# Performance work log

Measured on AMD Instinct MI355X. Metric: run time of the kernel, lower is better.

## Reference

```python
import jax, jax.numpy as jnp
import numpy as np

B, C, L, HEADS, DK = 32, 128, 32, 8, 64  # batch, channels, lattice side (L1=L2=L), heads, head dim
NLAYER = 4


def setup_inputs() -> dict:
    key = jax.random.key(0)
    ks = jax.random.split(key, 6)
    s_in = 1.0 / float(np.sqrt(C))          # lecun-normal scale for QKV (fan_in = channels)
    s_out = 1.0 / float(np.sqrt(HEADS * DK))  # lecun-normal scale for W0 (fan_in = dk*heads)
    return {
        "x": jax.random.normal(ks[0], (B, C, L, L), jnp.float32),
        "Wq": jax.random.normal(ks[1], (HEADS * DK, C), jnp.float32) * s_in,
        "Wk": jax.random.normal(ks[2], (HEADS * DK, C), jnp.float32) * s_in,
        "Wv": jax.random.normal(ks[3], (HEADS * DK, C), jnp.float32) * s_in,
        "R": jax.random.normal(ks[4], (HEADS, L, L), jnp.float32) * 0.02,
        "W0": jax.random.normal(ks[5], (C, HEADS * DK), jnp.float32) * s_out,
    }


def get_irpe(R):
    # r[h, i, j] = R[h, (xi - xj) mod L1, (yi - yj) mod L2]  (jnp negative indexing wraps)
    heads, L1, L2 = R.shape
    a1 = jnp.arange(L1)
    a2 = jnp.arange(L2)
    dx = (a1[:, None] - a1[None, :]) % L1        # (L1, L1)
    dy = (a2[:, None] - a2[None, :]) % L2        # (L2, L2)
    bias = R[:, dx[:, None, :, None], dy[None, :, None, :]]  # (heads, L1, L2, L1, L2)
    return bias.reshape(heads, L1 * L2, L1 * L2)


def reference(x, Wq, Wk, Wv, R, W0):
    bias = get_irpe(R)                            # (heads, N, N)
    inv_layer = 1.0 / float(np.sqrt(NLAYER + 1))
    inv_sqrt_dk = 1.0 / float(np.sqrt(DK))

    def block(xs):  # xs: (C, L, L) — single sample, as in the original __call__
        xn = xs * inv_layer
        xf = xn.reshape(C, -1)                    # (C, N)
        Q = (Wq @ xf).reshape(HEADS, DK, -1)      # 1x1 conv == matmul
        K = (Wk @ xf).reshape(HEADS, DK, -1)
        V = (Wv @ xf).reshape(HEADS, DK, -1)
        dot = jnp.einsum('hdi,hdj->hij', Q, K) + bias
        alpha = jax.nn.softmax(dot * inv_sqrt_dk, axis=-1)
        att = jnp.einsum('hij,hdj->hdi', alpha, V).reshape(HEADS * DK, -1)
        return (W0 @ att).reshape(xs.shape) + xs  # residual

    return jax.vmap(block)(x)
```

## Files before the change

### kernel.cpp

```cpp
#include <hip/hip_runtime.h>


#define NB   32
#define NH   8
#define SEQ  1024
#define DKH  64
#define HDIM 512
#define CIN  128

#define SCL 0.18033688011112042f

typedef __bf16 bf16x8 __attribute__((ext_vector_type(8)));
typedef float floatx4 __attribute__((ext_vector_type(4)));
typedef unsigned short u16x8 __attribute__((ext_vector_type(8)));
typedef unsigned int uintx4 __attribute__((ext_vector_type(4)));

__device__ __forceinline__ unsigned short f2bf(float f) {
    union { float f; unsigned int u; } c; c.f = f;
    unsigned int u = c.u;
    return (unsigned short)((u + 0x7fffu + ((u >> 16) & 1u)) >> 16);
}
__device__ __forceinline__ bf16x8 ldfrag(const unsigned short* p) {
    u16x8 v = *reinterpret_cast<const u16x8*>(p);
    return __builtin_bit_cast(bf16x8, v);
}
__device__ __forceinline__ unsigned int pkbf(float a, float b) {
    unsigned int ua = __builtin_bit_cast(unsigned int, a);
    unsigned int ub = __builtin_bit_cast(unsigned int, b);
    ua += 0x7fffu + ((ua >> 16) & 1u);
    ub += 0x7fffu + ((ub >> 16) & 1u);
    return __builtin_amdgcn_perm(ub, ua, 0x07060302u);
}
__device__ __forceinline__ unsigned int pkbf_t(float a, float b) {
    return __builtin_amdgcn_perm(__builtin_bit_cast(unsigned int, b),
                                 __builtin_bit_cast(unsigned int, a), 0x07060302u);
}


__global__ __launch_bounds__(256) void prep_wb(const float* __restrict__ Wq,
                                               const float* __restrict__ Wk,
                                               const float* __restrict__ Wv,
                                               const float* __restrict__ W0,
                                               const float* __restrict__ R,
                                               unsigned short* __restrict__ w2,
                                               unsigned short* __restrict__ w0f,
                                               float* __restrict__ biasG) {
    if (blockIdx.x < 256) {
        int gidx = blockIdx.x * 256 + threadIdx.x;
        int lane = gidx & 63, slot = gidx >> 6;
        int bb = slot & 1, a = (slot >> 1) & 1, dxx = (slot >> 2) & 31, h = slot >> 7;
        int q = lane >> 4, n = lane & 15;
        int iy = (a << 4) + n;
        const float* Rh = R + (h << 10) + (dxx << 5);
        floatx4 v;
        for (int r = 0; r < 4; ++r) {
            int jy = (bb << 4) + 4 * q + r;
            v[r] = Rh[(iy - jy) & 31] * SCL;
        }
        *(floatx4*)&biasG[(size_t)gidx * 4] = v;
    } else {
        int idx = (blockIdx.x - 256) * 256 + threadIdx.x;
        if (idx < 196608) {
            int row = idx >> 7, col = idx & 127;
            float v;
            if (row < 512)       v = Wq[idx] * SCL;
            else if (row < 1024) v = Wk[idx - 65536];
            else                 v = Wv[idx - 131072];
            int rt = row >> 4, nr = row & 15, kc = col >> 5, qc = (col & 31) >> 3, jc = col & 7;
            w2[((rt * 4 + kc) * 512) + (qc * 16 + nr) * 8 + jc] = f2bf(v);
        } else {
            int idx2 = idx - 196608;
            int row = idx2 >> 9, col = idx2 & 511;
            int rt = row >> 4, nr = row & 15, kcA = col >> 5, qc = (col & 31) >> 3, jc = col & 7;
            w0f[((rt * 16 + kcA) * 512) + (qc * 16 + nr) * 8 + jc] = f2bf(W0[idx2]);
        }
    }
}

__global__ __launch_bounds__(256) void prep_xt(const float* __restrict__ x,
                                               unsigned short* __restrict__ xt2) {
    __shared__ float lds[64 * 65];
    int b = blockIdx.x, c0 = blockIdx.y * 64, p0 = blockIdx.z * 64;
    int t = threadIdx.x, tr = t >> 6, tc = t & 63;
    const float inv_layer = 0.44721359549995793f;
    for (int rr = 0; rr < 16; ++rr) {
        int cl = rr * 4 + tr;
        lds[cl * 65 + tc] = x[(b * CIN + c0 + cl) * SEQ + p0 + tc];
    }
    __syncthreads();
    for (int rr = 0; rr < 16; ++rr) {
        int pl = rr * 4 + tr;
        int pos = p0 + pl, c = c0 + tc;
        int pt = pos >> 4, np = pos & 15, kc = c >> 5, qc = (c & 31) >> 3, jc = c & 7;
        xt2[((size_t)((b * 64 + pt) * 4 + kc) * 512) + (qc * 16 + np) * 8 + jc] =
            f2bf(lds[tc * 65 + pl] * inv_layer);
    }
}

__global__ __launch_bounds__(256, 4) void qkv_gemm(const unsigned short* __restrict__ xt2,
                                                   const unsigned short* __restrict__ w2,
                                                   unsigned short* __restrict__ Qt,
                                                   unsigned short* __restrict__ Kf,
                                                   unsigned short* __restrict__ Vf) {
    int b = blockIdx.x, y = blockIdx.y, zt = blockIdx.z;
    int tid = threadIdx.x, wave = tid >> 6, lane = tid & 63, q = lane >> 4, n = lane & 15;
    floatx4 acc[4];
    for (int s = 0; s < 4; ++s) acc[s] = (floatx4){0.f, 0.f, 0.f, 0.f};
    bf16x8 af[4], bfr[4][4];
    if (y < 16) {
        int rt = y * 4 + wave;
        const unsigned short* wbase = w2 + (size_t)rt * 4 * 512 + lane * 8;
        const unsigned short* xbase = xt2 + (size_t)(b * 64 + zt * 4) * 4 * 512 + lane * 8;
        for (int kc = 0; kc < 4; ++kc) af[kc] = ldfrag(wbase + kc * 512);
        for (int s = 0; s < 4; ++s)
            for (int kc = 0; kc < 4; ++kc) bfr[s][kc] = ldfrag(xbase + (s * 4 + kc) * 512);
        for (int kc = 0; kc < 4; ++kc)
            for (int s = 0; s < 4; ++s)
                acc[s] = __builtin_amdgcn_mfma_f32_16x16x32_bf16(af[kc], bfr[s][kc], acc[s], 0, 0, 0);
        int wrow0 = y * 64 + wave * 16;
        int pos0 = zt * 64;
        if (y < 8) {
            int h = wrow0 >> 6;
            int d0 = (wrow0 & 63) + 4 * q;
            for (int s = 0; s < 4; ++s) {
                uint2 pk;
                pk.x = pkbf(acc[s][0], acc[s][1]);
                pk.y = pkbf(acc[s][2], acc[s][3]);
                int pos = pos0 + 16 * s + n;
                *(uint2*)&Qt[((size_t)(b * NH + h) * SEQ + pos) * DKH + d0] = pk;
            }
        } else {
            int h = (wrow0 >> 6) - 8;
            int bh = b * NH + h;
            int cd = wave >> 1;
            int qk = 2 * (wave & 1) + (q >> 1);
            int jk = 4 * (q & 1);
            for (int s = 0; s < 4; ++s) {
                uint2 pk;
                pk.x = pkbf(acc[s][0], acc[s][1]);
                pk.y = pkbf(acc[s][2], acc[s][3]);
                size_t addr = ((size_t)(bh * 16 + zt) * 8 + s * 2 + cd) * 512
                              + (qk * 16 + n) * 8 + jk;
                *(uint2*)&Kf[addr] = pk;
            }
        }
    } else {
        int pt = zt * 4 + wave;
        const unsigned short* xbase = xt2 + (size_t)((b * 64 + pt) * 4) * 512 + lane * 8;
        int rtv0 = 64 + (y - 16) * 4;
        const unsigned short* wbase = w2 + (size_t)rtv0 * 4 * 512 + lane * 8;
        for (int kc = 0; kc < 4; ++kc) af[kc] = ldfrag(xbase + kc * 512);
        for (int s = 0; s < 4; ++s)
            for (int kc = 0; kc < 4; ++kc) bfr[s][kc] = ldfrag(wbase + (s * 4 + kc) * 512);
        for (int kc = 0; kc < 4; ++kc)
            for (int s = 0; s < 4; ++s)
                acc[s] = __builtin_amdgcn_mfma_f32_16x16x32_bf16(af[kc], bfr[s][kc], acc[s], 0, 0, 0);
        int vrow0 = (y - 16) * 64;
        int cj = wave >> 1;
        int jj0 = 4 * (wave & 1);
        for (int s = 0; s < 4; ++s) {
            int vrow = vrow0 + 16 * s + n;
            int h = vrow >> 6, d = vrow & 63;
            int u = d >> 4, nl = d & 15;
            uint2 pk;
            pk.x = pkbf(acc[s][0], acc[s][1]);
            pk.y = pkbf(acc[s][2], acc[s][3]);
            size_t addr = ((size_t)((b * NH + h) * 16 + zt) * 8 + u * 2 + cj) * 512
                          + (q * 16 + nl) * 8 + jj0;
            *(uint2*)&Vf[addr] = pk;
        }
    }
}

__global__ __launch_bounds__(256, 2) void attn_kernel(const unsigned short* __restrict__ Qt,
                                                      const unsigned short* __restrict__ Kf,
                                                      const unsigned short* __restrict__ Vf,
                                                      const float* __restrict__ biasG,
                                                      unsigned short* __restrict__ att2) {
    __shared__ alignas(16) unsigned short lds_k[2][8 * 512];
    __shared__ alignas(16) unsigned short lds_v[2][8 * 512];

    int gid = blockIdx.x;
    int bh = gid & 255, qb = gid >> 8;
    int b = bh >> 3, h = bh & 7;
    int tid = threadIdx.x, wave = tid >> 6, lane = tid & 63, q = lane >> 4, n = lane & 15;
    int i0 = qb * 256 + wave * 64;
    int ti0 = i0 >> 4;

    const unsigned short* qbase = Qt + (size_t)bh * SEQ * DKH;
    const unsigned short* kft = Kf + (size_t)bh * 16 * 4096;
    const unsigned short* vft = Vf + (size_t)bh * 16 * 4096;
    const float* bGh = biasG + ((size_t)h * 32 * 4 * 256) + lane * 4;

    bf16x8 aq[4][2];
    for (int qt = 0; qt < 4; ++qt)
        for (int c = 0; c < 2; ++c)
            aq[qt][c] = ldfrag(qbase + (i0 + 16 * qt + n) * DKH + c * 32 + q * 8);

    u16x8 ones_u;
    for (int t = 0; t < 8; ++t) ones_u[t] = 0x3F80;
    bf16x8 vone = __builtin_bit_cast(bf16x8, ones_u);

    floatx4 o[4][4], acc_l[4];
    for (int qt = 0; qt < 4; ++qt) {
        acc_l[qt] = (floatx4){0.f, 0.f, 0.f, 0.f};
        for (int u = 0; u < 4; ++u) o[qt][u] = (floatx4){0.f, 0.f, 0.f, 0.f};
    }

    {
        const unsigned short* kp = kft + tid * 16;
        const unsigned short* vp = vft + tid * 16;
        u16x8 k0 = *(const u16x8*)kp, k1 = *(const u16x8*)(kp + 8);
        u16x8 v0 = *(const u16x8*)vp, v1 = *(const u16x8*)(vp + 8);
        *(u16x8*)&lds_k[0][tid * 16]     = k0;
        *(u16x8*)&lds_k[0][tid * 16 + 8] = k1;
        *(u16x8*)&lds_v[0][tid * 16]     = v0;
        *(u16x8*)&lds_v[0][tid * 16 + 8] = v1;
    }
    __syncthreads();

    for (int kt = 0; kt < 16; ++kt) {
        int cur = kt & 1;
        u16x8 kpre0, kpre1, vpre0, vpre1;
        if (kt < 15) {
            const unsigned short* kp = kft + (kt + 1) * 4096 + tid * 16;
            const unsigned short* vp = vft + (kt + 1) * 4096 + tid * 16;
            kpre0 = *(const u16x8*)kp;  kpre1 = *(const u16x8*)(kp + 8);
            vpre0 = *(const u16x8*)vp;  vpre1 = *(const u16x8*)(vp + 8);
        }

        floatx4 bsv[4][4];
        for (int qt = 0; qt < 4; ++qt) {
            int tq = ti0 + qt;
            int a512 = (tq & 1) << 9;
            int e0 = (tq >> 1) - 2 * kt;
            for (int s = 0; s < 4; ++s) {
                int dxx = (e0 - (s >> 1)) & 31;
                bsv[qt][s] = *(const floatx4*)(bGh + (dxx << 10) + a512 + ((s & 1) << 8));
            }
        }

        bf16x8 kf2[4][2];
        for (int s = 0; s < 4; ++s)
            for (int c = 0; c < 2; ++c)
                kf2[s][c] = ldfrag(&lds_k[cur][(s * 2 + c) * 512 + lane * 8]);

        bf16x8 pf[4][2];
        for (int qt = 0; qt < 4; ++qt) {
            floatx4 sv[4];
            for (int s = 0; s < 4; ++s) {
                sv[s] = __builtin_amdgcn_mfma_f32_16x16x32_bf16(kf2[s][0], aq[qt][0], bsv[qt][s], 0, 0, 0);
                sv[s] = __builtin_amdgcn_mfma_f32_16x16x32_bf16(kf2[s][1], aq[qt][1], sv[s], 0, 0, 0);
            }
            for (int c = 0; c < 2; ++c) {
                uintx4 pu;
                pu[0] = pkbf_t(__builtin_amdgcn_exp2f(sv[2 * c][0]), __builtin_amdgcn_exp2f(sv[2 * c][1]));
                pu[1] = pkbf_t(__builtin_amdgcn_exp2f(sv[2 * c][2]), __builtin_amdgcn_exp2f(sv[2 * c][3]));
                pu[2] = pkbf_t(__builtin_amdgcn_exp2f(sv[2 * c + 1][0]), __builtin_amdgcn_exp2f(sv[2 * c + 1][1]));
                pu[3] = pkbf_t(__builtin_amdgcn_exp2f(sv[2 * c + 1][2]), __builtin_amdgcn_exp2f(sv[2 * c + 1][3]));
                pf[qt][c] = __builtin_bit_cast(bf16x8, pu);
            }
        }

        bf16x8 vf2[4][2];
        for (int u = 0; u < 4; ++u)
            for (int c = 0; c < 2; ++c)
                vf2[u][c] = ldfrag(&lds_v[cur][(u * 2 + c) * 512 + lane * 8]);
        for (int qt = 0; qt < 4; ++qt) {
            acc_l[qt] = __builtin_amdgcn_mfma_f32_16x16x32_bf16(vone, pf[qt][0], acc_l[qt], 0, 0, 0);
            acc_l[qt] = __builtin_amdgcn_mfma_f32_16x16x32_bf16(vone, pf[qt][1], acc_l[qt], 0, 0, 0);
        }
        for (int u = 0; u < 4; ++u)
            for (int qt = 0; qt < 4; ++qt) {
                o[qt][u] = __builtin_amdgcn_mfma_f32_16x16x32_bf16(vf2[u][0], pf[qt][0], o[qt][u], 0, 0, 0);
                o[qt][u] = __builtin_amdgcn_mfma_f32_16x16x32_bf16(vf2[u][1], pf[qt][1], o[qt][u], 0, 0, 0);
            }

        if (kt < 15) {
            int nxt = cur ^ 1;
            *(u16x8*)&lds_k[nxt][tid * 16]     = kpre0;
            *(u16x8*)&lds_k[nxt][tid * 16 + 8] = kpre1;
            *(u16x8*)&lds_v[nxt][tid * 16]     = vpre0;
            *(u16x8*)&lds_v[nxt][tid * 16 + 8] = vpre1;
        }
        __syncthreads();
    }

    for (int qt = 0; qt < 4; ++qt) {
        float inv = 1.0f / acc_l[qt][0];
        int pt = ti0 + qt;
        for (int u = 0; u < 4; ++u) {
            int kcA = 2 * h + (u >> 1);
            int q2 = 2 * (u & 1) + (q >> 1);
            uint2 pk;
            pk.x = pkbf(o[qt][u][0] * inv, o[qt][u][1] * inv);
            pk.y = pkbf(o[qt][u][2] * inv, o[qt][u][3] * inv);
            size_t addr = ((size_t)((b * 64 + pt) * 16 + kcA) * 512)
                          + (q2 * 16 + n) * 8 + 4 * (q & 1);
            *(uint2*)&att2[addr] = pk;
        }
    }
}

__global__ __launch_bounds__(256, 4) void out_gemm(const unsigned short* __restrict__ att2,
                                                   const unsigned short* __restrict__ w0f,
                                                   const float* __restrict__ x,
                                                   float* __restrict__ out) {
    int b = blockIdx.x, ct = blockIdx.y, ptb = blockIdx.z;
    int tid = threadIdx.x, wave = tid >> 6, lane = tid & 63, q = lane >> 4, n = lane & 15;
    int pos0 = ptb * 64 + wave * 16;
    int c0 = ct * 64;
    int pt = ptb * 4 + wave;
    const unsigned short* abase = att2 + (size_t)(b * 64 + pt) * 16 * 512 + lane * 8;
    const unsigned short* wbase = w0f + (size_t)(c0 >> 4) * 16 * 512 + lane * 8;
    floatx4 acc[4];
    for (int s = 0; s < 4; ++s) acc[s] = (floatx4){0.f, 0.f, 0.f, 0.f};
    for (int g = 0; g < 4; ++g) {
        bf16x8 af[4], bfr[4][4];
        for (int k2 = 0; k2 < 4; ++k2) af[k2] = ldfrag(abase + (g * 4 + k2) * 512);
        for (int s = 0; s < 4; ++s)
            for (int k2 = 0; k2 < 4; ++k2)
                bfr[s][k2] = ldfrag(wbase + (s * 16 + g * 4 + k2) * 512);
        for (int k2 = 0; k2 < 4; ++k2)
            for (int s = 0; s < 4; ++s)
                acc[s] = __builtin_amdgcn_mfma_f32_16x16x32_bf16(af[k2], bfr[s][k2], acc[s], 0, 0, 0);
    }
    int p0q = pos0 + 4 * q;
    for (int s = 0; s < 4; ++s) {
        int c = c0 + 16 * s + n;
        size_t idx = ((size_t)b * CIN + c) * SEQ + p0q;
        floatx4 res = *(const floatx4*)&x[idx];
        floatx4 v = acc[s] + res;
        *(floatx4*)&out[idx] = v;
    }
}

extern "C" void kernel_launch(void* const* d_in, const int* in_sizes, int n_in,
                              void* d_out, int out_size, void* d_ws, size_t ws_size,
                              hipStream_t stream) {
    const float* x  = (const float*)d_in[0];
    const float* Wq = (const float*)d_in[1];
    const float* Wk = (const float*)d_in[2];
    const float* Wv = (const float*)d_in[3];
    const float* R  = (const float*)d_in[4];
    const float* W0 = (const float*)d_in[5];
    float* out = (float*)d_out;

    char* ws = (char*)d_ws;
    size_t off = 0;
    unsigned short* Qt   = (unsigned short*)(ws + off); off += (size_t)NB * NH * SEQ * DKH * 2;
    unsigned short* Kf   = (unsigned short*)(ws + off); off += (size_t)NB * NH * SEQ * DKH * 2;
    unsigned short* Vf   = (unsigned short*)(ws + off); off += (size_t)NB * NH * SEQ * DKH * 2;
    unsigned short* att2 = (unsigned short*)(ws + off); off += (size_t)NB * SEQ * HDIM * 2;
    unsigned short* xt2  = (unsigned short*)(ws + off); off += (size_t)NB * SEQ * CIN * 2;
    unsigned short* w2   = (unsigned short*)(ws + off); off += (size_t)1536 * 128 * 2;
    unsigned short* w0f  = (unsigned short*)(ws + off); off += (size_t)128 * 512 * 2;
    float* biasG = (float*)(ws + off); off += (size_t)NH * 32 * 4 * 256 * 4;
    (void)ws_size; (void)in_sizes; (void)n_in; (void)out_size;

    prep_wb<<<1280, 256, 0, stream>>>(Wq, Wk, Wv, W0, R, w2, w0f, biasG);
    prep_xt<<<dim3(NB, 2, 16), 256, 0, stream>>>(x, xt2);
    qkv_gemm<<<dim3(NB, 24, 16), 256, 0, stream>>>(xt2, w2, Qt, Kf, Vf);
    attn_kernel<<<NB * NH * 4, 256, 0, stream>>>(Qt, Kf, Vf, biasG, att2);
    out_gemm<<<dim3(NB, 2, 16), 256, 0, stream>>>(att2, w0f, x, out);
}
```

Before: 219.0 us.

## Stream K/V and bias tiles into LDS via direct global-to-LDS loads

The attention kernel now prefetches the next K/V tiles with global_load_lds straight into the double-buffered LDS, so the data no longer passes through registers. It also keeps a ring buffer of relative-position bias tiles in LDS, since the bias tiles are shared across waves and iterations, replacing per-wave global bias reads. The QK, softmax and PV work is interleaved per query tile, with s_setprio around the MFMA groups. The two prep kernels are merged into a single launch. In exchange the attention kernel uses about 48KB more LDS, which may reduce occupancy, and the ring-buffer index arithmetic is intricate.

```diff
diff --git a/kernel.cpp b/kernel.cpp
--- a/kernel.cpp
+++ b/kernel.cpp
@@ -35,18 +35,26 @@
     return __builtin_amdgcn_perm(__builtin_bit_cast(unsigned int, b),
                                  __builtin_bit_cast(unsigned int, a), 0x07060302u);
 }
-
-
-__global__ __launch_bounds__(256) void prep_wb(const float* __restrict__ Wq,
-                                               const float* __restrict__ Wk,
-                                               const float* __restrict__ Wv,
-                                               const float* __restrict__ W0,
-                                               const float* __restrict__ R,
-                                               unsigned short* __restrict__ w2,
-                                               unsigned short* __restrict__ w0f,
-                                               float* __restrict__ biasG) {
-    if (blockIdx.x < 256) {
-        int gidx = blockIdx.x * 256 + threadIdx.x;
+__device__ __forceinline__ void g2l16(const void* g, void* l) {
+    __builtin_amdgcn_global_load_lds((const __attribute__((address_space(1))) void*)g,
+                                     (__attribute__((address_space(3))) void*)l, 16, 0, 0);
+}
+
+
+__global__ __launch_bounds__(256) void prep_all(const float* __restrict__ Wq,
+                                                const float* __restrict__ Wk,
+                                                const float* __restrict__ Wv,
+                                                const float* __restrict__ W0,
+                                                const float* __restrict__ R,
+                                                const float* __restrict__ x,
+                                                unsigned short* __restrict__ w2,
+                                                unsigned short* __restrict__ w0f,
+                                                float* __restrict__ biasG,
+                                                unsigned short* __restrict__ xt2) {
+    __shared__ float lds[64 * 65];
+    int bid = blockIdx.x;
+    if (bid < 256) {
+        int gidx = bid * 256 + threadIdx.x;
         int lane = gidx & 63, slot = gidx >> 6;
         int bb = slot & 1, a = (slot >> 1) & 1, dxx = (slot >> 2) & 31, h = slot >> 7;
         int q = lane >> 4, n = lane & 15;
@@ -58,8 +66,8 @@
             v[r] = Rh[(iy - jy) & 31] * SCL;
         }
         *(floatx4*)&biasG[(size_t)gidx * 4] = v;
-    } else {
-        int idx = (blockIdx.x - 256) * 256 + threadIdx.x;
+    } else if (bid < 1280) {
+        int idx = (bid - 256) * 256 + threadIdx.x;
         if (idx < 196608) {
             int row = idx >> 7, col = idx & 127;
             float v;
@@ -74,26 +82,24 @@
             int rt = row >> 4, nr = row & 15, kcA = col >> 5, qc = (col & 31) >> 3, jc = col & 7;
             w0f[((rt * 16 + kcA) * 512) + (qc * 16 + nr) * 8 + jc] = f2bf(W0[idx2]);
         }
-    }
-}
-
-__global__ __launch_bounds__(256) void prep_xt(const float* __restrict__ x,
-                                               unsigned short* __restrict__ xt2) {
-    __shared__ float lds[64 * 65];
-    int b = blockIdx.x, c0 = blockIdx.y * 64, p0 = blockIdx.z * 64;
-    int t = threadIdx.x, tr = t >> 6, tc = t & 63;
-    const float inv_layer = 0.44721359549995793f;
-    for (int rr = 0; rr < 16; ++rr) {
-        int cl = rr * 4 + tr;
-        lds[cl * 65 + tc] = x[(b * CIN + c0 + cl) * SEQ + p0 + tc];
-    }
-    __syncthreads();
-    for (int rr = 0; rr < 16; ++rr) {
-        int pl = rr * 4 + tr;
-        int pos = p0 + pl, c = c0 + tc;
-        int pt = pos >> 4, np = pos & 15, kc = c >> 5, qc = (c & 31) >> 3, jc = c & 7;
-        xt2[((size_t)((b * 64 + pt) * 4 + kc) * 512) + (qc * 16 + np) * 8 + jc] =
-            f2bf(lds[tc * 65 + pl] * inv_layer);
+    } else {
+        int r = bid - 1280;
+        int b = r & 31, yy = (r >> 5) & 1, zz = r >> 6;
+        int c0 = yy * 64, p0 = zz * 64;
+        int t = threadIdx.x, tr = t >> 6, tc = t & 63;
+        const float inv_layer = 0.44721359549995793f;
+        for (int rr = 0; rr < 16; ++rr) {
+            int cl = rr * 4 + tr;
+            lds[cl * 65 + tc] = x[(b * CIN + c0 + cl) * SEQ + p0 + tc];
+        }
+        __syncthreads();
+        for (int rr = 0; rr < 16; ++rr) {
+            int pl = rr * 4 + tr;
+            int pos = p0 + pl, c = c0 + tc;
+            int pt = pos >> 4, np = pos & 15, kc = c >> 5, qc = (c & 31) >> 3, jc = c & 7;
+            xt2[((size_t)((b * 64 + pt) * 4 + kc) * 512) + (qc * 16 + np) * 8 + jc] =
+                f2bf(lds[tc * 65 + pl] * inv_layer);
+        }
     }
 }
 
@@ -179,6 +185,7 @@
                                                       unsigned short* __restrict__ att2) {
     __shared__ alignas(16) unsigned short lds_k[2][8 * 512];
     __shared__ alignas(16) unsigned short lds_v[2][8 * 512];
+    __shared__ alignas(16) float lds_bias[12 * 1024];
 
     int gid = blockIdx.x;
     int bh = gid & 255, qb = gid >> 8;
@@ -190,7 +197,7 @@
     const unsigned short* qbase = Qt + (size_t)bh * SEQ * DKH;
     const unsigned short* kft = Kf + (size_t)bh * 16 * 4096;
     const unsigned short* vft = Vf + (size_t)bh * 16 * 4096;
-    const float* bGh = biasG + ((size_t)h * 32 * 4 * 256) + lane * 4;
+    const float* bGh = biasG + (size_t)h * 32768;
 
     bf16x8 aq[4][2];
     for (int qt = 0; qt < 4; ++qt)
@@ -207,82 +214,109 @@
         for (int u = 0; u < 4; ++u) o[qt][u] = (floatx4){0.f, 0.f, 0.f, 0.f};
     }
 
+    int wb64 = qb * 8 + 255;
+    int sbase = (qb * 8 + 47) % 12;
+    int abb = (wave >> 1) * 2 + (wave & 1);
+    int off0 = wave * 512;
+
     {
-        const unsigned short* kp = kft + tid * 16;
-        const unsigned short* vp = vft + tid * 16;
-        u16x8 k0 = *(const u16x8*)kp, k1 = *(const u16x8*)(kp + 8);
-        u16x8 v0 = *(const u16x8*)vp, v1 = *(const u16x8*)(vp + 8);
-        *(u16x8*)&lds_k[0][tid * 16]     = k0;
-        *(u16x8*)&lds_k[0][tid * 16 + 8] = k1;
-        *(u16x8*)&lds_v[0][tid * 16]     = v0;
-        *(u16x8*)&lds_v[0][tid * 16 + 8] = v1;
+        for (int rel = 0; rel < 9; ++rel) {
+            int dxx = (wb64 + rel) & 31;
+            int phys = sbase + rel; if (phys >= 12) phys -= 12;
+            g2l16(bGh + (dxx * 4 + abb) * 256 + lane * 4,
+                  &lds_bias[(phys * 4 + abb) * 256]);
+        }
+        g2l16(kft + off0 + lane * 8,        &lds_k[0][off0]);
+        g2l16(kft + 2048 + off0 + lane * 8, &lds_k[0][2048 + off0]);
+        g2l16(vft + off0 + lane * 8,        &lds_v[0][off0]);
+        g2l16(vft + 2048 + off0 + lane * 8, &lds_v[0][2048 + off0]);
     }
     __syncthreads();
 
     for (int kt = 0; kt < 16; ++kt) {
         int cur = kt & 1;
-        u16x8 kpre0, kpre1, vpre0, vpre1;
+        int t0 = sbase - 2; if (t0 < 0) t0 += 12;
+
         if (kt < 15) {
-            const unsigned short* kp = kft + (kt + 1) * 4096 + tid * 16;
-            const unsigned short* vp = vft + (kt + 1) * 4096 + tid * 16;
-            kpre0 = *(const u16x8*)kp;  kpre1 = *(const u16x8*)(kp + 8);
-            vpre0 = *(const u16x8*)vp;  vpre1 = *(const u16x8*)(vp + 8);
-        }
-
-        floatx4 bsv[4][4];
+            const unsigned short* kg = kft + (kt + 1) * 4096;
+            const unsigned short* vg = vft + (kt + 1) * 4096;
+            unsigned short* dk = &lds_k[cur ^ 1][0];
+            unsigned short* dv = &lds_v[cur ^ 1][0];
+            g2l16(kg + off0 + lane * 8,        dk + off0);
+            g2l16(kg + 2048 + off0 + lane * 8, dk + 2048 + off0);
+            g2l16(vg + off0 + lane * 8,        dv + off0);
+            g2l16(vg + 2048 + off0 + lane * 8, dv + 2048 + off0);
+            int t1 = t0 + 1; if (t1 >= 12) t1 -= 12;
+            int dx0 = (wb64 - 2) & 31;
+            int dx1 = (wb64 - 1) & 31;
+            g2l16(bGh + (dx0 * 4 + abb) * 256 + lane * 4,
+                  &lds_bias[(t0 * 4 + abb) * 256]);
+            g2l16(bGh + (dx1 * 4 + abb) * 256 + lane * 4,
+                  &lds_bias[(t1 * 4 + abb) * 256]);
+        }
+
+        int r0 = sbase + 2 * wave; if (r0 >= 12) r0 -= 12;
+        int r1 = r0 + 1; if (r1 >= 12) r1 -= 12;
+        int r2 = r0 + 2; if (r2 >= 12) r2 -= 12;
+        const float* pb0 = &lds_bias[r0 * 1024 + lane * 4];
+        const float* pb1 = &lds_bias[r1 * 1024 + lane * 4];
+        const float* pb2 = &lds_bias[r2 * 1024 + lane * 4];
+
+        bf16x8 kf2[4][2], vf2[4][2];
+#pragma unroll
+        for (int s = 0; s < 4; ++s)
+#pragma unroll
+            for (int c = 0; c < 2; ++c) {
+                kf2[s][c] = ldfrag(&lds_k[cur][(s * 2 + c) * 512 + lane * 8]);
+                vf2[s][c] = ldfrag(&lds_v[cur][(s * 2 + c) * 512 + lane * 8]);
+            }
+
+#pragma unroll
         for (int qt = 0; qt < 4; ++qt) {
-            int tq = ti0 + qt;
-            int a512 = (tq & 1) << 9;
-            int e0 = (tq >> 1) - 2 * kt;
-            for (int s = 0; s < 4; ++s) {
-                int dxx = (e0 - (s >> 1)) & 31;
-                bsv[qt][s] = *(const floatx4*)(bGh + (dxx << 10) + a512 + ((s & 1) << 8));
+            const float* bhi = (qt & 2) ? pb2 : pb1;
+            const float* blo = (qt & 2) ? pb1 : pb0;
+            const int aoff = (qt & 1) * 512;
+            floatx4 sv0 = *(const floatx4*)(bhi + aoff);
+            floatx4 sv1 = *(const floatx4*)(bhi + aoff + 256);
+            floatx4 sv2 = *(const floatx4*)(blo + aoff);
+            floatx4 sv3 = *(const floatx4*)(blo + aoff + 256);
+
+            __builtin_amdgcn_s_setprio(1);
+            sv0 = __builtin_amdgcn_mfma_f32_16x16x32_bf16(kf2[0][0], aq[qt][0], sv0, 0, 0, 0);
+            sv0 = __builtin_amdgcn_mfma_f32_16x16x32_bf16(kf2[0][1], aq[qt][1], sv0, 0, 0, 0);
+            sv1 = __builtin_amdgcn_mfma_f32_16x16x32_bf16(kf2[1][0], aq[qt][0], sv1, 0, 0, 0);
+            sv1 = __builtin_amdgcn_mfma_f32_16x16x32_bf16(kf2[1][1], aq[qt][1], sv1, 0, 0, 0);
+            sv2 = __builtin_amdgcn_mfma_f32_16x16x32_bf16(kf2[2][0], aq[qt][0], sv2, 0, 0, 0);
+            sv2 = __builtin_amdgcn_mfma_f32_16x16x32_bf16(kf2[2][1], aq[qt][1], sv2, 0, 0, 0);
+            sv3 = __builtin_amdgcn_mfma_f32_16x16x32_bf16(kf2[3][0], aq[qt][0], sv3, 0, 0, 0);
+            sv3 = __builtin_amdgcn_mfma_f32_16x16x32_bf16(kf2[3][1], aq[qt][1], sv3, 0, 0, 0);
+            __builtin_amdgcn_s_setprio(0);
+
+            uintx4 pu0, pu1;
+            pu0[0] = pkbf_t(__builtin_amdgcn_exp2f(sv0[0]), __builtin_amdgcn_exp2f(sv0[1]));
+            pu0[1] = pkbf_t(__builtin_amdgcn_exp2f(sv0[2]), __builtin_amdgcn_exp2f(sv0[3]));
+            pu0[2] = pkbf_t(__builtin_amdgcn_exp2f(sv1[0]), __builtin_amdgcn_exp2f(sv1[1]));
+            pu0[3] = pkbf_t(__builtin_amdgcn_exp2f(sv1[2]), __builtin_amdgcn_exp2f(sv1[3]));
+            pu1[0] = pkbf_t(__builtin_amdgcn_exp2f(sv2[0]), __builtin_amdgcn_exp2f(sv2[1]));
+            pu1[1] = pkbf_t(__builtin_amdgcn_exp2f(sv2[2]), __builtin_amdgcn_exp2f(sv2[3]));
+            pu1[2] = pkbf_t(__builtin_amdgcn_exp2f(sv3[0]), __builtin_amdgcn_exp2f(sv3[1]));
+            pu1[3] = pkbf_t(__builtin_amdgcn_exp2f(sv3[2]), __builtin_amdgcn_exp2f(sv3[3]));
+            bf16x8 pf0 = __builtin_bit_cast(bf16x8, pu0);
+            bf16x8 pf1 = __builtin_bit_cast(bf16x8, pu1);
+
+            __builtin_amdgcn_s_setprio(1);
+            acc_l[qt] = __builtin_amdgcn_mfma_f32_16x16x32_bf16(vone, pf0, acc_l[qt], 0, 0, 0);
+            acc_l[qt] = __builtin_amdgcn_mfma_f32_16x16x32_bf16(vone, pf1, acc_l[qt], 0, 0, 0);
+#pragma unroll
+            for (int u = 0; u < 4; ++u) {
+                o[qt][u] = __builtin_amdgcn_mfma_f32_16x16x32_bf16(vf2[u][0], pf0, o[qt][u], 0, 0, 0);
+                o[qt][u] = __builtin_amdgcn_mfma_f32_16x16x32_bf16(vf2[u][1], pf1, o[qt][u], 0, 0, 0);
             }
-        }
-
-        bf16x8 kf2[4][2];
-        for (int s = 0; s < 4; ++s)
-            for (int c = 0; c < 2; ++c)
-                kf2[s][c] = ldfrag(&lds_k[cur][(s * 2 + c) * 512 + lane * 8]);
-
-        bf16x8 pf[4][2];
-        for (int qt = 0; qt < 4; ++qt) {
-            floatx4 sv[4];
-            for (int s = 0; s < 4; ++s) {
-                sv[s] = __builtin_amdgcn_mfma_f32_16x16x32_bf16(kf2[s][0], aq[qt][0], bsv[qt][s], 0, 0, 0);
-                sv[s] = __builtin_amdgcn_mfma_f32_16x16x32_bf16(kf2[s][1], aq[qt][1], sv[s], 0, 0, 0);
-            }
-            for (int c = 0; c < 2; ++c) {
-                uintx4 pu;
-                pu[0] = pkbf_t(__builtin_amdgcn_exp2f(sv[2 * c][0]), __builtin_amdgcn_exp2f(sv[2 * c][1]));
-                pu[1] = pkbf_t(__builtin_amdgcn_exp2f(sv[2 * c][2]), __builtin_amdgcn_exp2f(sv[2 * c][3]));
-                pu[2] = pkbf_t(__builtin_amdgcn_exp2f(sv[2 * c + 1][0]), __builtin_amdgcn_exp2f(sv[2 * c + 1][1]));
-                pu[3] = pkbf_t(__builtin_amdgcn_exp2f(sv[2 * c + 1][2]), __builtin_amdgcn_exp2f(sv[2 * c + 1][3]));
-                pf[qt][c] = __builtin_bit_cast(bf16x8, pu);
-            }
-        }
-
-        bf16x8 vf2[4][2];
-        for (int u = 0; u < 4; ++u)
-            for (int c = 0; c < 2; ++c)
-                vf2[u][c] = ldfrag(&lds_v[cur][(u * 2 + c) * 512 + lane * 8]);
-        for (int qt = 0; qt < 4; ++qt) {
-            acc_l[qt] = __builtin_amdgcn_mfma_f32_16x16x32_bf16(vone, pf[qt][0], acc_l[qt], 0, 0, 0);
-            acc_l[qt] = __builtin_amdgcn_mfma_f32_16x16x32_bf16(vone, pf[qt][1], acc_l[qt], 0, 0, 0);
-        }
-        for (int u = 0; u < 4; ++u)
-            for (int qt = 0; qt < 4; ++qt) {
-                o[qt][u] = __builtin_amdgcn_mfma_f32_16x16x32_bf16(vf2[u][0], pf[qt][0], o[qt][u], 0, 0, 0);
-                o[qt][u] = __builtin_amdgcn_mfma_f32_16x16x32_bf16(vf2[u][1], pf[qt][1], o[qt][u], 0, 0, 0);
-            }
-
-        if (kt < 15) {
-            int nxt = cur ^ 1;
-            *(u16x8*)&lds_k[nxt][tid * 16]     = kpre0;
-            *(u16x8*)&lds_k[nxt][tid * 16 + 8] = kpre1;
-            *(u16x8*)&lds_v[nxt][tid * 16]     = vpre0;
-            *(u16x8*)&lds_v[nxt][tid * 16 + 8] = vpre1;
-        }
+            __builtin_amdgcn_s_setprio(0);
+        }
+
+        sbase = t0;
+        wb64 -= 2;
         __syncthreads();
     }
 
@@ -358,8 +392,7 @@
     float* biasG = (float*)(ws + off); off += (size_t)NH * 32 * 4 * 256 * 4;
     (void)ws_size; (void)in_sizes; (void)n_in; (void)out_size;
 
-    prep_wb<<<1280, 256, 0, stream>>>(Wq, Wk, Wv, W0, R, w2, w0f, biasG);
-    prep_xt<<<dim3(NB, 2, 16), 256, 0, stream>>>(x, xt2);
+    prep_all<<<2304, 256, 0, stream>>>(Wq, Wk, Wv, W0, R, x, w2, w0f, biasG, xt2);
     qkv_gemm<<<dim3(NB, 24, 16), 256, 0, stream>>>(xt2, w2, Qt, Kf, Vf);
     attn_kernel<<<NB * NH * 4, 256, 0, stream>>>(Qt, Kf, Vf, biasG, att2);
     out_gemm<<<dim3(NB, 2, 16), 256, 0, stream>>>(att2, w0f, x, out);
```

After: 208.6 us. -4.8%, faster.
